# Kernel optimization log

Measured on AMD Instinct MI355X. Metric: run time of the kernel, lower is better.

The kernel has to match this reference:

```python
import jax, jax.numpy as jnp
import numpy as np

K = 23          # tagset size
START = 21
STOP = 22
NEG = -10000.0
V, E, HH = 400000, 50, 128   # vocab, embed dim, per-direction hidden
T = 8192


def setup_inputs() -> dict:
    key = jax.random.key(0)
    ks = jax.random.split(key, 16)
    s = 1.0 / np.sqrt(HH)
    d = {
        "sentence": jax.random.randint(ks[0], (T,), 0, V, dtype=jnp.int32),
        "embed_table": jax.random.normal(ks[1], (V, E), jnp.float32),
        "Wih_f": jax.random.uniform(ks[2], (4 * HH, E), jnp.float32, -s, s),
        "Whh_f": jax.random.uniform(ks[3], (4 * HH, HH), jnp.float32, -s, s),
        "bih_f": jax.random.uniform(ks[4], (4 * HH,), jnp.float32, -s, s),
        "bhh_f": jax.random.uniform(ks[5], (4 * HH,), jnp.float32, -s, s),
        "Wih_b": jax.random.uniform(ks[6], (4 * HH, E), jnp.float32, -s, s),
        "Whh_b": jax.random.uniform(ks[7], (4 * HH, HH), jnp.float32, -s, s),
        "bih_b": jax.random.uniform(ks[8], (4 * HH,), jnp.float32, -s, s),
        "bhh_b": jax.random.uniform(ks[9], (4 * HH,), jnp.float32, -s, s),
        "W_out": jax.random.uniform(ks[10], (K, 2 * HH), jnp.float32, -s, s),
        "b_out": jax.random.uniform(ks[11], (K,), jnp.float32, -s, s),
        "transitions": jax.random.normal(ks[12], (K, K), jnp.float32),
        "h0": jax.random.normal(ks[13], (2, HH), jnp.float32),
        "c0": jax.random.normal(ks[14], (2, HH), jnp.float32),
    }
    return d


def _lstm_dir(x, Wih, Whh, bih, bhh, h0, c0, reverse):
    b = bih + bhh
    def step(carry, xt):
        h, c = carry
        g = Wih @ xt + Whh @ h + b            # [4*HH], gate order i,f,g,o
        i, f, gg, o = jnp.split(g, 4)
        i = jax.nn.sigmoid(i)
        f = jax.nn.sigmoid(f)
        gg = jnp.tanh(gg)
        o = jax.nn.sigmoid(o)
        c = f * c + i * gg
        h = o * jnp.tanh(c)
        return (h, c), h
    _, hs = jax.lax.scan(step, (h0, c0), x, reverse=reverse)
    return hs                                  # [T, HH], time-aligned


def _lstm_feats(sentence, embed_table, Wih_f, Whh_f, bih_f, bhh_f,
                Wih_b, Whh_b, bih_b, bhh_b, W_out, b_out, h0, c0):
    x = embed_table[sentence]                  # [T, E]
    hf = _lstm_dir(x, Wih_f, Whh_f, bih_f, bhh_f, h0[0], c0[0], False)
    hb = _lstm_dir(x, Wih_b, Whh_b, bih_b, bhh_b, h0[1], c0[1], True)
    h = jnp.concatenate([hf, hb], axis=-1)     # [T, 2*HH]
    return h @ W_out.T + b_out                 # [T, K]


def _constrained_transitions(transitions):
    t = transitions.at[START, :].set(NEG)      # nothing transitions into START
    t = t.at[:, STOP].set(NEG)                 # nothing transitions out of STOP
    return t


def _viterbi(feats, transitions):
    trans = _constrained_transitions(transitions)
    init = jnp.full((K,), NEG, feats.dtype).at[START].set(0.0)

    def step(fv, feat):
        scores = fv[None, :] + trans           # [K_next, K_prev]
        bptr = jnp.argmax(scores, axis=1)      # [K]
        fv_new = jnp.max(scores, axis=1) + feat
        return fv_new, bptr

    fv, bptrs = jax.lax.scan(step, init, feats)   # bptrs: [T, K]
    terminal = fv + trans[STOP]
    best_last = jnp.argmax(terminal)
    path_score = terminal[best_last]

    def back(tag, bp):
        prev = bp[tag]
        return prev, prev
    _, prevs = jax.lax.scan(back, best_last, bptrs, reverse=True)
    # prevs[t] = tag at time t-1; prevs[0] == START
    best_path = jnp.concatenate([prevs[1:], best_last[None]])  # [T]
    return path_score, best_path


def reference(sentence, embed_table, Wih_f, Whh_f, bih_f, bhh_f,
              Wih_b, Whh_b, bih_b, bhh_b, W_out, b_out,
              transitions, h0, c0):
    feats = _lstm_feats(sentence, embed_table, Wih_f, Whh_f, bih_f, bhh_f,
                        Wih_b, Whh_b, bih_b, bhh_b, W_out, b_out, h0, c0)
    score, tag_seq = _viterbi(feats, transitions)
    return score, tag_seq
```

## Files before the change

kernel.cpp:

```cpp
#include <hip/hip_runtime.h>

#define T_LEN 8192
#define HH 128
#define G4 512
#define E_DIM 50
#define KT 23
#define START_T 21
#define STOP_T 22
#define NEGV -10000.0f

__device__ __forceinline__ float rl(float v, int lane) {
  return __int_as_float(__builtin_amdgcn_readlane(__float_as_int(v), lane));
}

template <int CTRL>
__device__ __forceinline__ float dppmov(float x) {
  return __int_as_float(
      __builtin_amdgcn_mov_dpp(__float_as_int(x), CTRL, 0xF, 0xF, true));
}

__device__ __forceinline__ float xlane1(float x) { return dppmov<0xB1>(x); }
__device__ __forceinline__ float xlane2(float x) { return dppmov<0x4E>(x); }
__device__ __forceinline__ float xlane4(float x) { return dppmov<0x141>(dppmov<0x1B>(x)); }

__device__ __forceinline__ void pkfma(float2& acc, const float2 w, const float2 h) {
  asm volatile("v_pk_fma_f32 %0, %1, %2, %0" : "+v"(acc) : "v"(w), "v"(h));
}

template <int BURST>
__device__ __forceinline__ void ballast_spin(const int* flag, int target, float seed,
                                             float* sink) {
  float x = seed;
  const float aa = 1.0000001f, bb = 1e-7f;
  while (__hip_atomic_load(flag, __ATOMIC_RELAXED, __HIP_MEMORY_SCOPE_AGENT) < target) {
#pragma unroll
    for (int q = 0; q < BURST; ++q) x = fmaf(x, aa, bb);
  }
  if (x == 12345.678f) *sink = x;
}

__global__ __launch_bounds__(512) void k_pre(
    const int* __restrict__ sentence, const float* __restrict__ embed,
    const float* __restrict__ Wih_f, const float* __restrict__ bih_f, const float* __restrict__ bhh_f,
    const float* __restrict__ Wih_b, const float* __restrict__ bih_b, const float* __restrict__ bhh_b,
    float* __restrict__ pre_f, float* __restrict__ pre_b)
{
  const int dir = blockIdx.x >> 8;
  const int t0 = (blockIdx.x & 255) * 32;
  const float* __restrict__ Wih = dir ? Wih_b : Wih_f;
  const float* __restrict__ bi  = dir ? bih_b : bih_f;
  const float* __restrict__ bh  = dir ? bhh_b : bhh_f;
  float* __restrict__ pre = dir ? pre_b : pre_f;
  const int j = threadIdx.x;
  const int r = (((j >> 1) & 3) << 7) | ((j >> 3) << 1) | (j & 1);
  float w[E_DIM];
  {
    const float2* w2 = (const float2*)(Wih + r * E_DIM);
#pragma unroll
    for (int q = 0; q < 25; ++q) { float2 v = w2[q]; w[2*q] = v.x; w[2*q+1] = v.y; }
  }
  const float bias = bi[r] + bh[r];
  __shared__ float xs[32][E_DIM];
  __shared__ int sidx[32];
  if (j < 32) sidx[j] = sentence[t0 + j];
  __syncthreads();
  for (int i = j; i < 32 * E_DIM; i += 512) {
    int tl = i / E_DIM;
    int e = i - tl * E_DIM;
    xs[tl][e] = embed[sidx[tl] * E_DIM + e];
  }
  __syncthreads();
  for (int tl = 0; tl < 32; ++tl) {
    float a0 = bias, a1 = 0.f;
#pragma unroll
    for (int e = 0; e < E_DIM; e += 2) {
      a0 += w[e]     * xs[tl][e];
      a1 += w[e + 1] * xs[tl][e + 1];
    }
    pre[(t0 + tl) * G4 + j] = a0 + a1;
  }
}

__global__ __attribute__((amdgpu_flat_work_group_size(512, 512),
                          amdgpu_waves_per_eu(2, 2)))
void k_lstm(
    const float* __restrict__ Whh_f, const float* __restrict__ Whh_b,
    const float* __restrict__ h0, const float* __restrict__ c0,
    const float* __restrict__ pre_f, const float* __restrict__ pre_b,
    float* __restrict__ hcat, int* __restrict__ flag, float* __restrict__ sink)
{
  __shared__ float hbuf[2][HH];
  if (blockIdx.x >= 2) {
    if (threadIdx.x < 64)
      ballast_spin<512>(flag, 2, (float)(blockIdx.x * 64 + threadIdx.x), sink);
    return;
  }
  const int dir = blockIdx.x;
  const float* __restrict__ Whh = dir ? Whh_b : Whh_f;
  const float* __restrict__ pre = dir ? pre_b : pre_f;
  const int j = threadIdx.x;
  const int l = j & 7;
  const int O = j >> 3;
  const bool b0 = l & 1;
  const bool b1 = (l >> 1) & 1;
  const bool b2 = (l >> 2) & 1;
  const int g = (l >> 1) & 3;
  const int dim = (O << 1) | (l & 1);

  float2 wv[64];
#pragma unroll
  for (int i = 0; i < 8; ++i) {
    const int row = (((i >> 1) & 3) << 7) | (O << 1) | (i & 1);
    const float4* src = (const float4*)(Whh + row * HH);
#pragma unroll
    for (int k = 0; k < 4; ++k) {
      float4 v = src[l + 8 * k];
      wv[i * 8 + 2 * k]     = make_float2(v.x, v.y);
      wv[i * 8 + 2 * k + 1] = make_float2(v.z, v.w);
    }
  }
#define PIN8(B) asm volatile("" : "+v"(wv[B]), "+v"(wv[B+1]), "+v"(wv[B+2]), \
    "+v"(wv[B+3]), "+v"(wv[B+4]), "+v"(wv[B+5]), "+v"(wv[B+6]), "+v"(wv[B+7]))

  float c = c0[dir * HH + dim];
  if (g == 0) hbuf[0][dim] = h0[dir * HH + dim];
  __syncthreads();
  float pcur = pre[(dir ? (T_LEN - 1) : 0) * G4 + j];
  float pn1  = pre[(dir ? (T_LEN - 2) : 1) * G4 + j];

  for (int s = 0; s < T_LEN; ++s) {
    PIN8(0); PIN8(8); PIN8(16); PIN8(24); PIN8(32); PIN8(40); PIN8(48); PIN8(56);

    const int t  = dir ? (T_LEN - 1 - s) : s;
    const int s2i = (s + 2 < T_LEN) ? (s + 2) : (T_LEN - 1);
    const int t2 = dir ? (T_LEN - 1 - s2i) : s2i;
    const float pn2 = pre[t2 * G4 + j];

    const float4* h4 = (const float4*)hbuf[s & 1];
    const float4 hc0 = h4[l];
    const float4 hc1 = h4[l + 8];
    const float4 hc2 = h4[l + 16];
    const float4 hc3 = h4[l + 24];
    const float2 h0a = make_float2(hc0.x, hc0.y), h0b = make_float2(hc0.z, hc0.w);
    const float2 h1a = make_float2(hc1.x, hc1.y), h1b = make_float2(hc1.z, hc1.w);
    const float2 h2a = make_float2(hc2.x, hc2.y), h2b = make_float2(hc2.z, hc2.w);
    const float2 h3a = make_float2(hc3.x, hc3.y), h3b = make_float2(hc3.z, hc3.w);

    float2 acc[8];
#pragma unroll
    for (int i = 0; i < 8; ++i) {
      acc[i] = make_float2(0.f, 0.f);
      pkfma(acc[i], wv[i * 8 + 0], h0a);
      pkfma(acc[i], wv[i * 8 + 1], h0b);
      pkfma(acc[i], wv[i * 8 + 2], h1a);
      pkfma(acc[i], wv[i * 8 + 3], h1b);
      pkfma(acc[i], wv[i * 8 + 4], h2a);
      pkfma(acc[i], wv[i * 8 + 5], h2b);
      pkfma(acc[i], wv[i * 8 + 6], h3a);
      pkfma(acc[i], wv[i * 8 + 7], h3b);
    }
    const float p0 = acc[0].x + acc[0].y;
    const float p1 = acc[1].x + acc[1].y;
    const float p2 = acc[2].x + acc[2].y;
    const float p3 = acc[3].x + acc[3].y;
    const float p4 = acc[4].x + acc[4].y;
    const float p5 = acc[5].x + acc[5].y;
    const float p6 = acc[6].x + acc[6].y;
    const float p7 = acc[7].x + acc[7].y;

    const float u10 = b2 ? p4 : p0, v10 = b2 ? p0 : p4;
    const float u11 = b2 ? p5 : p1, v11 = b2 ? p1 : p5;
    const float u12 = b2 ? p6 : p2, v12 = b2 ? p2 : p6;
    const float u13 = b2 ? p7 : p3, v13 = b2 ? p3 : p7;
    const float q0 = u10 + xlane4(v10);
    const float q1 = u11 + xlane4(v11);
    const float q2 = u12 + xlane4(v12);
    const float q3 = u13 + xlane4(v13);
    const float u20 = b1 ? q2 : q0, v20 = b1 ? q0 : q2;
    const float u21 = b1 ? q3 : q1, v21 = b1 ? q1 : q3;
    const float r0 = u20 + xlane2(v20);
    const float r1 = u21 + xlane2(v21);
    const float u30 = b0 ? r1 : r0, v30 = b0 ? r0 : r1;
    const float dot = u30 + xlane1(v30);

    const float accv = dot + pcur;
    pcur = pn1; pn1 = pn2;

    const float sc = (g == 2) ? 2.0f : 1.0f;
    const float ev = __expf(-sc * accv);
    const float sg = 1.0f / (1.0f + ev);
    const float a  = (g == 2) ? (2.0f * sg - 1.0f) : sg;
    const float s2v = xlane2(a);
    const float s4v = xlane4(a);
    const float s6v = xlane2(s4v);
    const float iv  = b2 ? (b1 ? s6v : s4v) : (b1 ? s2v : a);
    const float fv  = b2 ? (b1 ? s4v : s6v) : (b1 ? a   : s2v);
    const float gv  = b2 ? (b1 ? s2v : a  ) : (b1 ? s6v : s4v);
    const float ovv = b2 ? (b1 ? a   : s2v) : (b1 ? s4v : s6v);
    c = fv * c + iv * gv;
    const float e2 = __expf(-2.0f * c);
    const float th = 2.0f / (1.0f + e2) - 1.0f;
    const float h = ovv * th;
    if (g == 0) {
      hbuf[(s + 1) & 1][dim] = h;
      hcat[t * (2 * HH) + dir * HH + dim] = h;
    }
    __syncthreads();
  }
#undef PIN8
  if (j == 0) atomicAdd(flag, 1);
}

__global__ __launch_bounds__(256) void k_feats(
    const float* __restrict__ hcat, const float* __restrict__ Wout,
    const float* __restrict__ bout, float* __restrict__ feats32)
{
  const int t0 = blockIdx.x * 32;
  __shared__ float hsh[32 * 257];
  __shared__ float wsh[KT * 256];
  __shared__ float bsh[KT];
  const int tid = threadIdx.x;
  for (int i = tid; i < 32 * 256; i += 256) {
    int tl = i >> 8, dd = i & 255;
    hsh[tl * 257 + dd] = hcat[(t0 + tl) * 256 + dd];
  }
  for (int i = tid; i < KT * 256; i += 256) wsh[i] = Wout[i];
  if (tid < KT) bsh[tid] = bout[tid];
  __syncthreads();
  for (int idx = tid; idx < 32 * KT; idx += 256) {
    int tl = idx & 31, k = idx >> 5;
    float a0 = bsh[k], a1 = 0.f, a2 = 0.f, a3 = 0.f;
#pragma unroll 8
    for (int dd = 0; dd < 256; dd += 4) {
      a0 += hsh[tl * 257 + dd + 0] * wsh[k * 256 + dd + 0];
      a1 += hsh[tl * 257 + dd + 1] * wsh[k * 256 + dd + 1];
      a2 += hsh[tl * 257 + dd + 2] * wsh[k * 256 + dd + 2];
      a3 += hsh[tl * 257 + dd + 3] * wsh[k * 256 + dd + 3];
    }
    feats32[(t0 + tl) * 32 + k] = ((a0 + a1) + (a2 + a3));
  }
}

__global__ __launch_bounds__(64) void k_vit_fwd(
    const float* __restrict__ feats32, const float* __restrict__ trans,
    float* __restrict__ fvstore, float* __restrict__ out, int* __restrict__ misc,
    int* __restrict__ flag, float* __restrict__ sink)
{
  if (blockIdx.x >= 1) {
    ballast_spin<256>(flag, 1, (float)(blockIdx.x * 64 + threadIdx.x), sink);
    return;
  }
  const int j = threadIdx.x;
  const int j32 = j & 31;
  float trow[KT];
#pragma unroll
  for (int i = 0; i < KT; ++i)
    trow[i] = (j < KT) ? ((j == START_T || i == STOP_T) ? NEGV : trans[j * KT + i]) : NEGV;
  float fvn = (j == START_T) ? 0.0f : NEGV;
  float pf[8];
#pragma unroll
  for (int q = 0; q < 8; ++q) pf[q] = feats32[q * 32 + j32];

#define MAX3(a,b,cc) fmaxf(fmaxf((a),(b)),(cc))
#define CAND(i) (rl(fvn, (i)) + trow[(i)])

  for (int tb = 0; tb < T_LEN; tb += 8) {
#pragma unroll
    for (int q = 0; q < 8; ++q) {
      const int t = tb + q;
      fvstore[t * 64 + j] = fvn;
      float m0 = MAX3(CAND(0),  CAND(1),  CAND(2));
      float m1 = MAX3(CAND(3),  CAND(4),  CAND(5));
      float m2 = MAX3(CAND(6),  CAND(7),  CAND(8));
      float m3 = MAX3(CAND(9),  CAND(10), CAND(11));
      float m4 = MAX3(CAND(12), CAND(13), CAND(14));
      float m5 = MAX3(CAND(15), CAND(16), CAND(17));
      float m6 = MAX3(CAND(18), CAND(19), CAND(20));
      float m7 = fmaxf(CAND(21), CAND(22));
      float n0 = MAX3(m0, m1, m2);
      float n1 = MAX3(m3, m4, m5);
      float n2 = fmaxf(m6, m7);
      const float best = MAX3(n0, n1, n2);
      fvn = best + pf[q];
      const int tpf = t + 8;
      const int tc = (tpf < T_LEN) ? tpf : (T_LEN - 1);
      pf[q] = feats32[tc * 32 + j32];
    }
  }
  const float trS = (j < KT) ? ((j == STOP_T) ? NEGV : trans[STOP_T * KT + j]) : 0.0f;
  float term = (j < KT) ? (fvn + trS) : -3.0e38f;
  int idx = (j < KT) ? j : 63;
#pragma unroll
  for (int off = 16; off >= 1; off >>= 1) {
    float ovl = __shfl_xor(term, off);
    int oi = __shfl_xor(idx, off);
    if (ovl > term || (ovl == term && oi < idx)) { term = ovl; idx = oi; }
  }
  if (j == 0) { out[0] = term; misc[0] = idx; atomicAdd(flag, 1); }
}

__global__ __launch_bounds__(256) void k_bptr(
    const float* __restrict__ fvstore, const float* __restrict__ trans,
    unsigned char* __restrict__ bptr)
{
  const int t0 = blockIdx.x * 32;
  __shared__ float fv[32 * 24];
  __shared__ float trc[KT * KT];
  const int tid = threadIdx.x;
  for (int i = tid; i < 32 * 24; i += 256) {
    int tl = i / 24, e = i - tl * 24;
    fv[i] = fvstore[(t0 + tl) * 64 + e];
  }
  for (int i = tid; i < KT * KT; i += 256) {
    int jj = i / KT, ii = i - jj * KT;
    trc[i] = (jj == START_T || ii == STOP_T) ? NEGV : trans[i];
  }
  __syncthreads();
  for (int p = tid; p < 32 * KT; p += 256) {
    int tl = p / KT, jj = p - tl * KT;
    const float* fvr = fv + tl * 24;
    const float* tr = trc + jj * KT;
    float best = fvr[0] + tr[0]; int bi = 0;
#pragma unroll
    for (int i = 1; i < KT; ++i) {
      float v = fvr[i] + tr[i];
      if (v > best) { best = v; bi = i; }
    }
    bptr[(t0 + tl) * KT + jj] = (unsigned char)bi;
  }
}

__global__ __launch_bounds__(64) void k_compose(
    const unsigned char* __restrict__ bptr, unsigned char* __restrict__ maps)
{
  const int c = blockIdx.x;
  const int lo = c * 32;
  __shared__ unsigned char rows[32 * 24];
  const int tid = threadIdx.x;
  for (int i = tid; i < 32 * KT; i += 64) {
    int tl = i / KT, e = i - tl * KT;
    rows[tl * 24 + e] = bptr[(lo + tl) * KT + e];
  }
  __syncthreads();
  if (tid < KT) {
    int x = tid;
    for (int tl = 31; tl >= 0; --tl) x = rows[tl * 24 + x];
    maps[c * KT + tid] = (unsigned char)x;
  }
}

__global__ __launch_bounds__(64) void k_backscan(
    const unsigned char* __restrict__ maps, const int* __restrict__ misc,
    int* __restrict__ btags)
{
  __shared__ unsigned char msh[256 * KT];
  const int tid = threadIdx.x;
  for (int i = tid; i < 256 * KT; i += 64) msh[i] = maps[i];
  __syncthreads();
  if (tid == 0) {
    int e = misc[0];
    for (int c = 255; c >= 0; --c) { btags[c] = e; e = msh[c * KT + e]; }
  }
}

__global__ __launch_bounds__(64) void k_backeval(
    const unsigned char* __restrict__ bptr, const int* __restrict__ btags,
    float* __restrict__ out)
{
  const int c = blockIdx.x;
  const int lo = c * 32;
  __shared__ unsigned char rows[32 * 24];
  __shared__ int tags[32];
  const int tid = threadIdx.x;
  for (int i = tid; i < 32 * KT; i += 64) {
    int tl = i / KT, e = i - tl * KT;
    rows[tl * 24 + e] = bptr[(lo + tl) * KT + e];
  }
  __syncthreads();
  if (tid == 0) {
    int tg = btags[c];
    tags[31] = tg;
    for (int tl = 31; tl >= 1; --tl) { tg = rows[tl * 24 + tg]; tags[tl - 1] = tg; }
  }
  __syncthreads();
  if (tid < 32) out[1 + lo + tid] = (float)tags[tid];
}

extern "C" void kernel_launch(void* const* d_in, const int* in_sizes, int n_in,
                              void* d_out, int out_size, void* d_ws, size_t ws_size,
                              hipStream_t stream) {
  const int*   sentence = (const int*)d_in[0];
  const float* embed    = (const float*)d_in[1];
  const float* Wih_f    = (const float*)d_in[2];
  const float* Whh_f    = (const float*)d_in[3];
  const float* bih_f    = (const float*)d_in[4];
  const float* bhh_f    = (const float*)d_in[5];
  const float* Wih_b    = (const float*)d_in[6];
  const float* Whh_b    = (const float*)d_in[7];
  const float* bih_b    = (const float*)d_in[8];
  const float* bhh_b    = (const float*)d_in[9];
  const float* Wout     = (const float*)d_in[10];
  const float* bout     = (const float*)d_in[11];
  const float* trans    = (const float*)d_in[12];
  const float* h0       = (const float*)d_in[13];
  const float* c0       = (const float*)d_in[14];
  float* out = (float*)d_out;

  float* ws = (float*)d_ws;
  float* pre_f = ws;
  float* pre_b = pre_f + (size_t)T_LEN * G4;
  float* hcat  = pre_b + (size_t)T_LEN * G4;
  float* feats32 = hcat + (size_t)T_LEN * 2 * HH;
  unsigned char* bptr = (unsigned char*)(feats32 + (size_t)T_LEN * 32);
  unsigned char* maps = bptr + (size_t)T_LEN * KT;
  int* btags = (int*)(maps + 256 * KT);
  int* misc  = btags + 256;
  int* flags = misc + 8;
  float* sink = (float*)(flags + 8);
  float* fvstore = pre_f;

  hipMemsetAsync(flags, 0, 8 * sizeof(int), stream);
  k_pre<<<512, 512, 0, stream>>>(sentence, embed, Wih_f, bih_f, bhh_f,
                                 Wih_b, bih_b, bhh_b, pre_f, pre_b);
  k_lstm<<<256, 512, 0, stream>>>(Whh_f, Whh_b, h0, c0, pre_f, pre_b, hcat,
                                  flags + 0, sink);
  k_feats<<<256, 256, 0, stream>>>(hcat, Wout, bout, feats32);
  k_vit_fwd<<<256, 64, 0, stream>>>(feats32, trans, fvstore, out, misc,
                                    flags + 1, sink);
  k_bptr<<<256, 256, 0, stream>>>(fvstore, trans, bptr);
  k_compose<<<256, 64, 0, stream>>>(bptr, maps);
  k_backscan<<<1, 64, 0, stream>>>(maps, misc, btags);
  k_backeval<<<256, 64, 0, stream>>>(bptr, btags, out);
}
```

Measured before the change: 7.641 ms.

## Unroll LSTM recurrence by 8 with batched prefetch, lightweight barrier, deferred hcat stores

Restructures the serial LSTM recurrence loop into 8-step unrolled blocks with double-buffered register arrays of precomputed input projections, loaded one block ahead. Global hcat stores are deferred to the end of each block, and __syncthreads is replaced by an explicit LDS waitcnt plus s_barrier with a sched_barrier. Packed FMA inline asm is replaced by scalar fmaf so the compiler can schedule freely. The goal is to shorten the per-step critical path by moving global memory traffic and vmcnt waits off each barrier. The cost is higher register pressure alongside the 128-register weight cache.

```diff
diff --git a/kernel.cpp b/kernel.cpp
--- a/kernel.cpp
+++ b/kernel.cpp
@@ -23,9 +23,16 @@
 __device__ __forceinline__ float xlane2(float x) { return dppmov<0x4E>(x); }
 __device__ __forceinline__ float xlane4(float x) { return dppmov<0x141>(dppmov<0x1B>(x)); }
 
-__device__ __forceinline__ void pkfma(float2& acc, const float2 w, const float2 h) {
-  asm volatile("v_pk_fma_f32 %0, %1, %2, %0" : "+v"(acc) : "v"(w), "v"(h));
-}
+__device__ __forceinline__ void cfma(float2& acc, const float2 w, const float2 h) {
+  acc.x = fmaf(w.x, h.x, acc.x);
+  acc.y = fmaf(w.y, h.y, acc.y);
+}
+
+#define LSTM_BARRIER() do {                                   \
+    asm volatile("s_waitcnt lgkmcnt(0)" ::: "memory");        \
+    __builtin_amdgcn_s_barrier();                             \
+    __builtin_amdgcn_sched_barrier(0);                        \
+  } while (0)
 
 template <int BURST>
 __device__ __forceinline__ void ballast_spin(const int* flag, int target, float seed,
@@ -121,93 +128,108 @@
   }
 #define PIN8(B) asm volatile("" : "+v"(wv[B]), "+v"(wv[B+1]), "+v"(wv[B+2]), \
     "+v"(wv[B+3]), "+v"(wv[B+4]), "+v"(wv[B+5]), "+v"(wv[B+6]), "+v"(wv[B+7]))
+  PIN8(0); PIN8(8); PIN8(16); PIN8(24); PIN8(32); PIN8(40); PIN8(48); PIN8(56);
+#undef PIN8
 
   float c = c0[dir * HH + dim];
   if (g == 0) hbuf[0][dim] = h0[dir * HH + dim];
   __syncthreads();
-  float pcur = pre[(dir ? (T_LEN - 1) : 0) * G4 + j];
-  float pn1  = pre[(dir ? (T_LEN - 2) : 1) * G4 + j];
-
-  for (int s = 0; s < T_LEN; ++s) {
-    PIN8(0); PIN8(8); PIN8(16); PIN8(24); PIN8(32); PIN8(40); PIN8(48); PIN8(56);
-
-    const int t  = dir ? (T_LEN - 1 - s) : s;
-    const int s2i = (s + 2 < T_LEN) ? (s + 2) : (T_LEN - 1);
-    const int t2 = dir ? (T_LEN - 1 - s2i) : s2i;
-    const float pn2 = pre[t2 * G4 + j];
-
-    const float4* h4 = (const float4*)hbuf[s & 1];
-    const float4 hc0 = h4[l];
-    const float4 hc1 = h4[l + 8];
-    const float4 hc2 = h4[l + 16];
-    const float4 hc3 = h4[l + 24];
-    const float2 h0a = make_float2(hc0.x, hc0.y), h0b = make_float2(hc0.z, hc0.w);
-    const float2 h1a = make_float2(hc1.x, hc1.y), h1b = make_float2(hc1.z, hc1.w);
-    const float2 h2a = make_float2(hc2.x, hc2.y), h2b = make_float2(hc2.z, hc2.w);
-    const float2 h3a = make_float2(hc3.x, hc3.y), h3b = make_float2(hc3.z, hc3.w);
-
-    float2 acc[8];
-#pragma unroll
-    for (int i = 0; i < 8; ++i) {
-      acc[i] = make_float2(0.f, 0.f);
-      pkfma(acc[i], wv[i * 8 + 0], h0a);
-      pkfma(acc[i], wv[i * 8 + 1], h0b);
-      pkfma(acc[i], wv[i * 8 + 2], h1a);
-      pkfma(acc[i], wv[i * 8 + 3], h1b);
-      pkfma(acc[i], wv[i * 8 + 4], h2a);
-      pkfma(acc[i], wv[i * 8 + 5], h2b);
-      pkfma(acc[i], wv[i * 8 + 6], h3a);
-      pkfma(acc[i], wv[i * 8 + 7], h3b);
-    }
-    const float p0 = acc[0].x + acc[0].y;
-    const float p1 = acc[1].x + acc[1].y;
-    const float p2 = acc[2].x + acc[2].y;
-    const float p3 = acc[3].x + acc[3].y;
-    const float p4 = acc[4].x + acc[4].y;
-    const float p5 = acc[5].x + acc[5].y;
-    const float p6 = acc[6].x + acc[6].y;
-    const float p7 = acc[7].x + acc[7].y;
-
-    const float u10 = b2 ? p4 : p0, v10 = b2 ? p0 : p4;
-    const float u11 = b2 ? p5 : p1, v11 = b2 ? p1 : p5;
-    const float u12 = b2 ? p6 : p2, v12 = b2 ? p2 : p6;
-    const float u13 = b2 ? p7 : p3, v13 = b2 ? p3 : p7;
-    const float q0 = u10 + xlane4(v10);
-    const float q1 = u11 + xlane4(v11);
-    const float q2 = u12 + xlane4(v12);
-    const float q3 = u13 + xlane4(v13);
-    const float u20 = b1 ? q2 : q0, v20 = b1 ? q0 : q2;
-    const float u21 = b1 ? q3 : q1, v21 = b1 ? q1 : q3;
-    const float r0 = u20 + xlane2(v20);
-    const float r1 = u21 + xlane2(v21);
-    const float u30 = b0 ? r1 : r0, v30 = b0 ? r0 : r1;
-    const float dot = u30 + xlane1(v30);
-
-    const float accv = dot + pcur;
-    pcur = pn1; pn1 = pn2;
-
-    const float sc = (g == 2) ? 2.0f : 1.0f;
-    const float ev = __expf(-sc * accv);
-    const float sg = 1.0f / (1.0f + ev);
-    const float a  = (g == 2) ? (2.0f * sg - 1.0f) : sg;
-    const float s2v = xlane2(a);
-    const float s4v = xlane4(a);
-    const float s6v = xlane2(s4v);
-    const float iv  = b2 ? (b1 ? s6v : s4v) : (b1 ? s2v : a);
-    const float fv  = b2 ? (b1 ? s4v : s6v) : (b1 ? a   : s2v);
-    const float gv  = b2 ? (b1 ? s2v : a  ) : (b1 ? s6v : s4v);
-    const float ovv = b2 ? (b1 ? a   : s2v) : (b1 ? s4v : s6v);
-    c = fv * c + iv * gv;
-    const float e2 = __expf(-2.0f * c);
-    const float th = 2.0f / (1.0f + e2) - 1.0f;
-    const float h = ovv * th;
-    if (g == 0) {
-      hbuf[(s + 1) & 1][dim] = h;
-      hcat[t * (2 * HH) + dir * HH + dim] = h;
-    }
-    __syncthreads();
-  }
-#undef PIN8
+
+#define TIX(s) (dir ? (T_LEN - 1 - (s)) : (s))
+  float pf[8], pg[8];
+#pragma unroll
+  for (int q = 0; q < 8; ++q) pf[q] = pre[TIX(q) * G4 + j];
+
+#define BLOCK8(PF, PG, SB) {                                                  \
+    const int nb_ = (SB) + 8;                                                 \
+    if (nb_ < T_LEN) {                                                        \
+      _Pragma("unroll")                                                       \
+      for (int q = 0; q < 8; ++q) PG[q] = pre[TIX(nb_ + q) * G4 + j];         \
+    }                                                                         \
+    float hst[8];                                                             \
+    _Pragma("unroll")                                                         \
+    for (int q = 0; q < 8; ++q) {                                             \
+      const int s = (SB) + q;                                                 \
+      const float4* h4 = (const float4*)hbuf[s & 1];                          \
+      const float4 hc0 = h4[l];                                               \
+      const float4 hc1 = h4[l + 8];                                           \
+      const float4 hc2 = h4[l + 16];                                          \
+      const float4 hc3 = h4[l + 24];                                          \
+      const float2 h0a = make_float2(hc0.x, hc0.y);                           \
+      const float2 h0b = make_float2(hc0.z, hc0.w);                           \
+      const float2 h1a = make_float2(hc1.x, hc1.y);                           \
+      const float2 h1b = make_float2(hc1.z, hc1.w);                           \
+      const float2 h2a = make_float2(hc2.x, hc2.y);                           \
+      const float2 h2b = make_float2(hc2.z, hc2.w);                           \
+      const float2 h3a = make_float2(hc3.x, hc3.y);                           \
+      const float2 h3b = make_float2(hc3.z, hc3.w);                           \
+      float2 acc[8];                                                          \
+      _Pragma("unroll")                                                       \
+      for (int i = 0; i < 8; ++i) {                                           \
+        acc[i] = make_float2(0.f, 0.f);                                       \
+        cfma(acc[i], wv[i * 8 + 0], h0a);                                     \
+        cfma(acc[i], wv[i * 8 + 1], h0b);                                     \
+        cfma(acc[i], wv[i * 8 + 2], h1a);                                     \
+        cfma(acc[i], wv[i * 8 + 3], h1b);                                     \
+        cfma(acc[i], wv[i * 8 + 4], h2a);                                     \
+        cfma(acc[i], wv[i * 8 + 5], h2b);                                     \
+        cfma(acc[i], wv[i * 8 + 6], h3a);                                     \
+        cfma(acc[i], wv[i * 8 + 7], h3b);                                     \
+      }                                                                       \
+      const float p0 = acc[0].x + acc[0].y;                                   \
+      const float p1 = acc[1].x + acc[1].y;                                   \
+      const float p2 = acc[2].x + acc[2].y;                                   \
+      const float p3 = acc[3].x + acc[3].y;                                   \
+      const float p4 = acc[4].x + acc[4].y;                                   \
+      const float p5 = acc[5].x + acc[5].y;                                   \
+      const float p6 = acc[6].x + acc[6].y;                                   \
+      const float p7 = acc[7].x + acc[7].y;                                   \
+      const float u10 = b2 ? p4 : p0, v10 = b2 ? p0 : p4;                     \
+      const float u11 = b2 ? p5 : p1, v11 = b2 ? p1 : p5;                     \
+      const float u12 = b2 ? p6 : p2, v12 = b2 ? p2 : p6;                     \
+      const float u13 = b2 ? p7 : p3, v13 = b2 ? p3 : p7;                     \
+      const float q0 = u10 + xlane4(v10);                                     \
+      const float q1 = u11 + xlane4(v11);                                     \
+      const float q2 = u12 + xlane4(v12);                                     \
+      const float q3 = u13 + xlane4(v13);                                     \
+      const float r0 = (b1 ? q2 : q0) + xlane2(b1 ? q0 : q2);                 \
+      const float r1 = (b1 ? q3 : q1) + xlane2(b1 ? q1 : q3);                 \
+      const float dot = (b0 ? r1 : r0) + xlane1(b0 ? r0 : r1);                \
+      const float accv = dot + PF[q];                                         \
+      const float sc = (g == 2) ? 2.0f : 1.0f;                                \
+      const float ev = __expf(-sc * accv);                                    \
+      const float sg = 1.0f / (1.0f + ev);                                    \
+      const float a  = (g == 2) ? (2.0f * sg - 1.0f) : sg;                    \
+      const float s2v = xlane2(a);                                            \
+      const float s4v = xlane4(a);                                            \
+      const float s6v = xlane2(s4v);                                          \
+      const float iv  = b2 ? (b1 ? s6v : s4v) : (b1 ? s2v : a);               \
+      const float fv  = b2 ? (b1 ? s4v : s6v) : (b1 ? a   : s2v);             \
+      const float gv  = b2 ? (b1 ? s2v : a  ) : (b1 ? s6v : s4v);             \
+      const float ovv = b2 ? (b1 ? a   : s2v) : (b1 ? s4v : s6v);             \
+      c = fv * c + iv * gv;                                                   \
+      const float e2 = __expf(-2.0f * c);                                     \
+      const float th = 2.0f / (1.0f + e2) - 1.0f;                             \
+      const float h = ovv * th;                                               \
+      if (g == 0) {                                                           \
+        hbuf[(s + 1) & 1][dim] = h;                                           \
+        hst[q] = h;                                                           \
+      }                                                                       \
+      LSTM_BARRIER();                                                         \
+    }                                                                         \
+    if (g == 0) {                                                             \
+      _Pragma("unroll")                                                       \
+      for (int q = 0; q < 8; ++q)                                             \
+        hcat[TIX((SB) + q) * (2 * HH) + dir * HH + dim] = hst[q];             \
+    }                                                                         \
+  }
+
+  for (int sb = 0; sb < T_LEN; sb += 16) {
+    BLOCK8(pf, pg, sb);
+    BLOCK8(pg, pf, sb + 8);
+  }
+#undef BLOCK8
+#undef TIX
   if (j == 0) atomicAdd(flag, 1);
 }
 
```

Measured after the change: 6.434 ms. -15.8%, faster.
